# Kernel tuning notes

Hardware: AMD Instinct MI355X
Metric: run time of the kernel (lower is better)

Reference implementation:

```python
import jax, jax.numpy as jnp
import numpy as np

B, N, MAX_V = 256, 16384, 64

def setup_inputs() -> dict:
    key = jax.random.key(0)
    ks = jax.random.split(key, 11)
    s = 0.02
    x = jax.random.normal(ks[0], (B, N, 5), dtype=jnp.float32)
    W1 = jax.random.normal(ks[1], (2, 32), dtype=jnp.float32) * s
    b1 = jnp.zeros((32,), jnp.float32)
    W2 = jax.random.normal(ks[2], (32, 64), dtype=jnp.float32) * s
    b2 = jnp.zeros((64,), jnp.float32)
    W3 = jax.random.normal(ks[3], (201, 256), dtype=jnp.float32) * s
    b3 = jnp.zeros((256,), jnp.float32)
    W4 = jax.random.normal(ks[4], (256, 128), dtype=jnp.float32) * s
    b4 = jnp.zeros((128,), jnp.float32)
    W5 = jax.random.normal(ks[5], (128, MAX_V * 4), dtype=jnp.float32) * s
    # existence-logit biases initialized to -2.0 (indices i*4+3)
    b5 = jnp.zeros((MAX_V * 4,), jnp.float32).at[jnp.arange(MAX_V) * 4 + 3].set(-2.0)
    return {"x": x, "W1": W1, "b1": b1, "W2": W2, "b2": b2,
            "W3": W3, "b3": b3, "W4": W4, "b4": b4, "W5": W5, "b5": b5}

def _pca_align(coords):
    # coords: [B,N,3]
    n = coords.shape[1]
    centroid = coords.mean(axis=1, keepdims=True)          # [B,1,3]
    centered = coords - centroid                           # [B,N,3]
    cov = jnp.einsum('bni,bnj->bij', centered, centered) / n
    evals, evecs = jnp.linalg.eigh(cov)                    # ascending
    evals = evals[:, ::-1]                                 # descending
    evecs = evecs[:, :, ::-1]
    # det sign fix on 3rd column
    det = jnp.linalg.det(evecs)
    evecs = evecs.at[:, :, 2].multiply(jnp.where(det < 0, -1.0, 1.0)[:, None])
    # deterministic sign: each axis points toward side with more mass (vectorized)
    proj = jnp.einsum('bnd,bde->bne', centered, evecs)     # [B,N,3]
    pos = (proj > 0).sum(axis=1)
    neg = (proj < 0).sum(axis=1)
    sign = jnp.where(neg > pos, -1.0, 1.0)                 # [B,3]
    evecs = evecs * sign[:, None, :]
    aligned = jnp.einsum('bnd,bde->bne', centered, evecs)  # [B,N,3]
    eig_norm = evals / (evals.sum(axis=1, keepdims=True) + 1e-8)
    extents = aligned.max(axis=1) - aligned.min(axis=1)    # [B,3]
    pca_features = jnp.concatenate([eig_norm, extents, centroid[:, 0]], axis=1)  # [B,9]
    return aligned, pca_features, evecs, centroid

def reference(x, W1, b1, W2, b2, W3, b3, W4, b4, W5, b5):
    coords = x[:, :, :3]
    sem = x[:, :, 3:]                                      # [B,N,2]
    aligned, pca_features, rot, centroid = _pca_align(coords)
    # per-point MLP
    pf = jax.nn.relu(sem @ W1 + b1)
    pf = jax.nn.relu(pf @ W2 + b2)                         # [B,N,64]
    gmax = pf.max(axis=1)
    gavg = pf.mean(axis=1)
    gstd = jnp.std(pf, axis=1, ddof=1)                     # torch.std is unbiased
    g = jnp.concatenate([gmax, gavg, gstd, pca_features], axis=1)  # [B,201]
    h = jax.nn.relu(g @ W3 + b3)
    h = jax.nn.relu(h @ W4 + b4)
    out = (h @ W5 + b5).reshape(x.shape[0], MAX_V, 4)      # [B,64,4]
    return out
```

## Files before the change

kernel.cpp:

```cpp
#include <hip/hip_runtime.h>
#include <math.h>

#define BATCH 256
#define NPTS  16384
#define TPB   256

#define P1_CHUNKS     8
#define P1_PTS_BLOCK  (NPTS / P1_CHUNKS)
#define P1_ITERS      8

#define PART_STRIDE 256

typedef __bf16 bf16x8  __attribute__((ext_vector_type(8)));
typedef float  floatx4 __attribute__((ext_vector_type(4)));

__global__ __launch_bounds__(TPB, 4)
void pass1_kernel(const float* __restrict__ x, const float* __restrict__ W1,
                  const float* __restrict__ b1, const float* __restrict__ W2,
                  const float* __restrict__ b2, float* __restrict__ ws) {
    const int b     = blockIdx.x;
    const int chunk = blockIdx.y;
    const int tid   = threadIdx.x;
    const int lane  = tid & 63;
    const int wave  = tid >> 6;
    const int quad  = lane >> 4;
    const int l15   = lane & 15;

    bf16x8 Bf[4];
    float  b2n[4];
#pragma unroll
    for (int t = 0; t < 4; ++t) {
        int n = t * 16 + l15;
#pragma unroll
        for (int j = 0; j < 8; ++j)
            Bf[t][j] = (__bf16)W2[(quad * 8 + j) * 64 + n];
        b2n[t] = b2[n];
    }
    float w1a[8], w1b[8], b1r[8];
#pragma unroll
    for (int j = 0; j < 8; ++j) {
        int jj = quad * 8 + j;
        w1a[j] = W1[jj];
        w1b[j] = W1[32 + jj];
        b1r[j] = b1[jj];
    }

    float vmax[4] = {0.f, 0.f, 0.f, 0.f};
    float vsum[4] = {0.f, 0.f, 0.f, 0.f};
    float vsq[4]  = {0.f, 0.f, 0.f, 0.f};
    float mo[9];
#pragma unroll
    for (int j = 0; j < 9; ++j) mo[j] = 0.f;

    const float* xb = x + ((size_t)b * NPTS + (size_t)chunk * P1_PTS_BLOCK) * 5;

    for (int it = 0; it < P1_ITERS; ++it) {
        const int pbase = wave * (P1_ITERS * 64) + it * 64;
        const float* p = xb + (size_t)(pbase + lane) * 5;
        float c0 = p[0], c1 = p[1], c2 = p[2], s0 = p[3], s1 = p[4];
        mo[0] += c0; mo[1] += c1; mo[2] += c2;
        mo[3] = fmaf(c0, c0, mo[3]); mo[4] = fmaf(c0, c1, mo[4]); mo[5] = fmaf(c0, c2, mo[5]);
        mo[6] = fmaf(c1, c1, mo[6]); mo[7] = fmaf(c1, c2, mo[7]); mo[8] = fmaf(c2, c2, mo[8]);

#pragma unroll
        for (int g = 0; g < 4; ++g) {
            int src = g * 16 + l15;
            float gs0 = __shfl(s0, src);
            float gs1 = __shfl(s1, src);
            bf16x8 Af;
#pragma unroll
            for (int j = 0; j < 8; ++j) {
                float v = fmaf(gs0, w1a[j], fmaf(gs1, w1b[j], b1r[j]));
                Af[j] = (__bf16)fmaxf(v, 0.f);
            }
#pragma unroll
            for (int t = 0; t < 4; ++t) {
                floatx4 C = {b2n[t], b2n[t], b2n[t], b2n[t]};
                C = __builtin_amdgcn_mfma_f32_16x16x32_bf16(Af, Bf[t], C, 0, 0, 0);
#pragma unroll
                for (int r = 0; r < 4; ++r) {
                    float v = fmaxf(C[r], 0.f);
                    vmax[t] = fmaxf(vmax[t], v);
                    vsum[t] += v;
                    vsq[t]  = fmaf(v, v, vsq[t]);
                }
            }
        }
    }

#pragma unroll
    for (int t = 0; t < 4; ++t) {
        vmax[t] = fmaxf(vmax[t], __shfl_xor(vmax[t], 16));
        vmax[t] = fmaxf(vmax[t], __shfl_xor(vmax[t], 32));
        vsum[t] += __shfl_xor(vsum[t], 16);
        vsum[t] += __shfl_xor(vsum[t], 32);
        vsq[t]  += __shfl_xor(vsq[t], 16);
        vsq[t]  += __shfl_xor(vsq[t], 32);
    }
#pragma unroll
    for (int j = 0; j < 9; ++j) {
        float v = mo[j];
#pragma unroll
        for (int o = 32; o > 0; o >>= 1) v += __shfl_xor(v, o);
        mo[j] = v;
    }

    __shared__ float red[4][201];
    if (quad == 0) {
#pragma unroll
        for (int t = 0; t < 4; ++t) {
            red[wave][t * 16 + l15]       = vmax[t];
            red[wave][64 + t * 16 + l15]  = vsum[t];
            red[wave][128 + t * 16 + l15] = vsq[t];
        }
    }
    if (lane == 0) {
#pragma unroll
        for (int j = 0; j < 9; ++j) red[wave][192 + j] = mo[j];
    }
    __syncthreads();

    if (tid < 201) {
        float v0 = red[0][tid], v1 = red[1][tid], v2 = red[2][tid], v3 = red[3][tid];
        float r = (tid < 64) ? fmaxf(fmaxf(v0, v1), fmaxf(v2, v3))
                             : (v0 + v1) + (v2 + v3);
        ws[(size_t)(b * P1_CHUNKS + chunk) * PART_STRIDE + tid] = r;
    }
}

__global__ __launch_bounds__(TPB)
void mid_kernel(const float* __restrict__ x,
                const float* __restrict__ W3, const float* __restrict__ b3,
                const float* __restrict__ W4, const float* __restrict__ b4,
                const float* __restrict__ W5, const float* __restrict__ b5,
                const float* __restrict__ ws, float* __restrict__ out) {
    const int b = blockIdx.x, t = threadIdx.x;
    const int lane = t & 63, wave = t >> 6;

    __shared__ float comb[201];
    __shared__ float eg[15];
    __shared__ float redmm[4][8];
    __shared__ float g[224];
    __shared__ float h1[256];
    __shared__ float h2[128];

    if (t < 201) {
        const float* base = ws + (size_t)b * P1_CHUNKS * PART_STRIDE + t;
        float acc = base[0];
        if (t < 64) {
#pragma unroll
            for (int i = 1; i < P1_CHUNKS; ++i) acc = fmaxf(acc, base[i * PART_STRIDE]);
        } else {
#pragma unroll
            for (int i = 1; i < P1_CHUNKS; ++i) acc += base[i * PART_STRIDE];
        }
        comb[t] = acc;
    }
    __syncthreads();

    if (t == 0) {
        const float n = (float)NPTS;
        float mx = comb[192] / n, my = comb[193] / n, mz = comb[194] / n;
        float A[3][3];
        A[0][0] = comb[195] / n - mx * mx; A[0][1] = comb[196] / n - mx * my;
        A[0][2] = comb[197] / n - mx * mz;
        A[1][1] = comb[198] / n - my * my; A[1][2] = comb[199] / n - my * mz;
        A[2][2] = comb[200] / n - mz * mz;
        A[1][0] = A[0][1]; A[2][0] = A[0][2]; A[2][1] = A[1][2];
        float V[3][3] = {{1, 0, 0}, {0, 1, 0}, {0, 0, 1}};
        const int PP[3] = {0, 0, 1};
        const int QQ[3] = {1, 2, 2};
        for (int sweep = 0; sweep < 7; ++sweep) {
            for (int r3 = 0; r3 < 3; ++r3) {
                int p = PP[r3], q = QQ[r3];
                float apq = A[p][q];
                if (fabsf(apq) < 1e-35f) continue;
                float theta = (A[q][q] - A[p][p]) / (2.0f * apq);
                float tt = 1.0f / (fabsf(theta) + sqrtf(fmaf(theta, theta, 1.0f)));
                if (theta < 0.0f) tt = -tt;
                float c = 1.0f / sqrtf(fmaf(tt, tt, 1.0f)), s = tt * c;
                float apq_t = tt * apq;
                A[p][p] -= apq_t;
                A[q][q] += apq_t;
                A[p][q] = A[q][p] = 0.0f;
                for (int r = 0; r < 3; ++r) {
                    if (r != p && r != q) {
                        float arp = A[r][p], arq = A[r][q];
                        A[r][p] = A[p][r] = c * arp - s * arq;
                        A[r][q] = A[q][r] = s * arp + c * arq;
                    }
                    float vrp = V[r][p], vrq = V[r][q];
                    V[r][p] = c * vrp - s * vrq;
                    V[r][q] = s * vrp + c * vrq;
                }
            }
        }
        float w[3] = {A[0][0], A[1][1], A[2][2]};
        int i0 = 0, i1 = 1, i2 = 2, sw;
        if (w[i0] < w[i1]) { sw = i0; i0 = i1; i1 = sw; }
        if (w[i0] < w[i2]) { sw = i0; i0 = i2; i2 = sw; }
        if (w[i1] < w[i2]) { sw = i1; i1 = i2; i2 = sw; }
        int idx[3] = {i0, i1, i2};
        for (int e = 0; e < 3; ++e)
            for (int comp = 0; comp < 3; ++comp)
                eg[e * 3 + comp] = V[comp][idx[e]];
        float sum = w[0] + w[1] + w[2] + 1e-8f;
        for (int e = 0; e < 3; ++e) eg[9 + e] = w[idx[e]] / sum;
        eg[12] = mx; eg[13] = my; eg[14] = mz;
    }
    __syncthreads();

    float e0x = eg[0], e0y = eg[1], e0z = eg[2];
    float e1x = eg[3], e1y = eg[4], e1z = eg[5];
    float e2x = eg[6], e2y = eg[7], e2z = eg[8];
    float cx = eg[12], cy = eg[13], cz = eg[14];

    const float* xb = x + (size_t)b * NPTS * 5;
    float mn[3] = {3.4e38f, 3.4e38f, 3.4e38f};
    float mx3[3] = {-3.4e38f, -3.4e38f, -3.4e38f};
#pragma unroll 4
    for (int i = 0; i < NPTS / TPB; ++i) {
        const float* p = xb + (size_t)(i * TPB + t) * 5;
        float c0 = p[0] - cx, c1 = p[1] - cy, c2 = p[2] - cz;
        float p0 = fmaf(c0, e0x, fmaf(c1, e0y, c2 * e0z));
        float p1 = fmaf(c0, e1x, fmaf(c1, e1y, c2 * e1z));
        float p2 = fmaf(c0, e2x, fmaf(c1, e2y, c2 * e2z));
        mn[0] = fminf(mn[0], p0); mx3[0] = fmaxf(mx3[0], p0);
        mn[1] = fminf(mn[1], p1); mx3[1] = fmaxf(mx3[1], p1);
        mn[2] = fminf(mn[2], p2); mx3[2] = fmaxf(mx3[2], p2);
    }
#pragma unroll
    for (int d = 0; d < 3; ++d) {
        float v = mx3[d];
#pragma unroll
        for (int o = 32; o > 0; o >>= 1) v = fmaxf(v, __shfl_xor(v, o));
        if (lane == 0) redmm[wave][d] = v;
        float u = mn[d];
#pragma unroll
        for (int o = 32; o > 0; o >>= 1) u = fminf(u, __shfl_xor(u, o));
        if (lane == 0) redmm[wave][4 + d] = u;
    }
    __syncthreads();

    if (t < 64) {
        g[t] = comb[t];
        float s = comb[64 + t], sq = comb[128 + t];
        float avg = s * (1.0f / NPTS);
        g[64 + t] = avg;
        float var = (sq - s * avg) / (float)(NPTS - 1);
        g[128 + t] = sqrtf(fmaxf(var, 0.f));
    } else if (t < 73) {
        int j = t - 64;
        if (j < 3) {
            g[192 + j] = eg[9 + j];
        } else if (j < 6) {
            int d = j - 3;
            float fmx = fmaxf(fmaxf(redmm[0][d], redmm[1][d]), fmaxf(redmm[2][d], redmm[3][d]));
            float fmn = fminf(fminf(redmm[0][4 + d], redmm[1][4 + d]),
                              fminf(redmm[2][4 + d], redmm[3][4 + d]));
            g[195 + d] = fmx - fmn;
        } else {
            g[198 + (j - 6)] = eg[12 + (j - 6)];
        }
    }
    __syncthreads();

    float a = b3[t];
    for (int j = 0; j < 201; ++j) a = fmaf(g[j], W3[j * 256 + t], a);
    h1[t] = fmaxf(a, 0.f);
    __syncthreads();
    if (t < 128) {
        float a2 = b4[t];
        for (int j = 0; j < 256; ++j) a2 = fmaf(h1[j], W4[j * 128 + t], a2);
        h2[t] = fmaxf(a2, 0.f);
    }
    __syncthreads();
    float o = b5[t];
    for (int j = 0; j < 128; ++j) o = fmaf(h2[j], W5[j * 256 + t], o);
    out[(size_t)b * 256 + t] = o;
}

extern "C" void kernel_launch(void* const* d_in, const int* in_sizes, int n_in,
                              void* d_out, int out_size, void* d_ws, size_t ws_size,
                              hipStream_t stream) {
    const float* x  = (const float*)d_in[0];
    const float* W1 = (const float*)d_in[1];
    const float* b1 = (const float*)d_in[2];
    const float* W2 = (const float*)d_in[3];
    const float* b2 = (const float*)d_in[4];
    const float* W3 = (const float*)d_in[5];
    const float* b3 = (const float*)d_in[6];
    const float* W4 = (const float*)d_in[7];
    const float* b4 = (const float*)d_in[8];
    const float* W5 = (const float*)d_in[9];
    const float* b5 = (const float*)d_in[10];
    float* out = (float*)d_out;
    float* ws  = (float*)d_ws;

    pass1_kernel<<<dim3(BATCH, P1_CHUNKS), TPB, 0, stream>>>(x, W1, b1, W2, b2, ws);
    mid_kernel<<<dim3(BATCH), TPB, 0, stream>>>(x, W3, b3, W4, b4, W5, b5, ws, out);
}
```

Measured before the change: 224.3 us.

## Fuse pass1 and head kernels using last-block-arrives atomic counter per batch

Merges the per-point pass and the per-batch head kernel into one launch: each chunk block writes its partials, bumps a per-batch atomic counter, and the last arriving block does the PCA, extent scan and MLP head. A tiny kernel zeroes the counters first. This removes the wait between the two kernels so head work for one batch can overlap other batches' pass1 blocks. In exchange it adds an extra launch, fences and atomics, and enlarges shared memory and registers in the fused kernel, which may lower occupancy.

```diff
diff --git a/kernel.cpp b/kernel.cpp
--- a/kernel.cpp
+++ b/kernel.cpp
@@ -10,14 +10,23 @@
 #define P1_ITERS      8
 
 #define PART_STRIDE 256
+#define COUNTER_OFF (BATCH * P1_CHUNKS * PART_STRIDE)
 
 typedef __bf16 bf16x8  __attribute__((ext_vector_type(8)));
 typedef float  floatx4 __attribute__((ext_vector_type(4)));
 
+__global__ void init_counters_kernel(unsigned* __restrict__ wsu) {
+    wsu[COUNTER_OFF + threadIdx.x] = 0u;
+}
+
 __global__ __launch_bounds__(TPB, 4)
-void pass1_kernel(const float* __restrict__ x, const float* __restrict__ W1,
+void fused_kernel(const float* __restrict__ x, const float* __restrict__ W1,
                   const float* __restrict__ b1, const float* __restrict__ W2,
-                  const float* __restrict__ b2, float* __restrict__ ws) {
+                  const float* __restrict__ b2,
+                  const float* __restrict__ W3, const float* __restrict__ b3,
+                  const float* __restrict__ W4, const float* __restrict__ b4,
+                  const float* __restrict__ W5, const float* __restrict__ b5,
+                  float* __restrict__ ws, float* __restrict__ out) {
     const int b     = blockIdx.x;
     const int chunk = blockIdx.y;
     const int tid   = threadIdx.x;
@@ -126,17 +135,19 @@
                              : (v0 + v1) + (v2 + v3);
         ws[(size_t)(b * P1_CHUNKS + chunk) * PART_STRIDE + tid] = r;
     }
-}
-
-__global__ __launch_bounds__(TPB)
-void mid_kernel(const float* __restrict__ x,
-                const float* __restrict__ W3, const float* __restrict__ b3,
-                const float* __restrict__ W4, const float* __restrict__ b4,
-                const float* __restrict__ W5, const float* __restrict__ b5,
-                const float* __restrict__ ws, float* __restrict__ out) {
-    const int b = blockIdx.x, t = threadIdx.x;
-    const int lane = t & 63, wave = t >> 6;
-
+
+    __threadfence();
+    __syncthreads();
+    __shared__ unsigned arrival;
+    if (tid == 0) {
+        unsigned* cnt = (unsigned*)ws + COUNTER_OFF + b;
+        arrival = atomicAdd(cnt, 1u);
+    }
+    __syncthreads();
+    if (arrival != P1_CHUNKS - 1) return;
+    __threadfence();
+
+    const int lane2 = tid & 63, wave2 = tid >> 6;
     __shared__ float comb[201];
     __shared__ float eg[15];
     __shared__ float redmm[4][8];
@@ -144,21 +155,21 @@
     __shared__ float h1[256];
     __shared__ float h2[128];
 
-    if (t < 201) {
-        const float* base = ws + (size_t)b * P1_CHUNKS * PART_STRIDE + t;
+    if (tid < 201) {
+        volatile const float* base = ws + (size_t)b * P1_CHUNKS * PART_STRIDE + tid;
         float acc = base[0];
-        if (t < 64) {
+        if (tid < 64) {
 #pragma unroll
             for (int i = 1; i < P1_CHUNKS; ++i) acc = fmaxf(acc, base[i * PART_STRIDE]);
         } else {
 #pragma unroll
             for (int i = 1; i < P1_CHUNKS; ++i) acc += base[i * PART_STRIDE];
         }
-        comb[t] = acc;
-    }
-    __syncthreads();
-
-    if (t == 0) {
+        comb[tid] = acc;
+    }
+    __syncthreads();
+
+    if (tid == 0) {
         const float n = (float)NPTS;
         float mx = comb[192] / n, my = comb[193] / n, mz = comb[194] / n;
         float A[3][3];
@@ -215,12 +226,12 @@
     float e2x = eg[6], e2y = eg[7], e2z = eg[8];
     float cx = eg[12], cy = eg[13], cz = eg[14];
 
-    const float* xb = x + (size_t)b * NPTS * 5;
+    const float* xf = x + (size_t)b * NPTS * 5;
     float mn[3] = {3.4e38f, 3.4e38f, 3.4e38f};
     float mx3[3] = {-3.4e38f, -3.4e38f, -3.4e38f};
 #pragma unroll 4
     for (int i = 0; i < NPTS / TPB; ++i) {
-        const float* p = xb + (size_t)(i * TPB + t) * 5;
+        const float* p = xf + (size_t)(i * TPB + tid) * 5;
         float c0 = p[0] - cx, c1 = p[1] - cy, c2 = p[2] - cz;
         float p0 = fmaf(c0, e0x, fmaf(c1, e0y, c2 * e0z));
         float p1 = fmaf(c0, e1x, fmaf(c1, e1y, c2 * e1z));
@@ -234,23 +245,23 @@
         float v = mx3[d];
 #pragma unroll
         for (int o = 32; o > 0; o >>= 1) v = fmaxf(v, __shfl_xor(v, o));
-        if (lane == 0) redmm[wave][d] = v;
+        if (lane2 == 0) redmm[wave2][d] = v;
         float u = mn[d];
 #pragma unroll
         for (int o = 32; o > 0; o >>= 1) u = fminf(u, __shfl_xor(u, o));
-        if (lane == 0) redmm[wave][4 + d] = u;
-    }
-    __syncthreads();
-
-    if (t < 64) {
-        g[t] = comb[t];
-        float s = comb[64 + t], sq = comb[128 + t];
+        if (lane2 == 0) redmm[wave2][4 + d] = u;
+    }
+    __syncthreads();
+
+    if (tid < 64) {
+        g[tid] = comb[tid];
+        float s = comb[64 + tid], sq = comb[128 + tid];
         float avg = s * (1.0f / NPTS);
-        g[64 + t] = avg;
+        g[64 + tid] = avg;
         float var = (sq - s * avg) / (float)(NPTS - 1);
-        g[128 + t] = sqrtf(fmaxf(var, 0.f));
-    } else if (t < 73) {
-        int j = t - 64;
+        g[128 + tid] = sqrtf(fmaxf(var, 0.f));
+    } else if (tid < 73) {
+        int j = tid - 64;
         if (j < 3) {
             g[192 + j] = eg[9 + j];
         } else if (j < 6) {
@@ -265,19 +276,19 @@
     }
     __syncthreads();
 
-    float a = b3[t];
-    for (int j = 0; j < 201; ++j) a = fmaf(g[j], W3[j * 256 + t], a);
-    h1[t] = fmaxf(a, 0.f);
-    __syncthreads();
-    if (t < 128) {
-        float a2 = b4[t];
-        for (int j = 0; j < 256; ++j) a2 = fmaf(h1[j], W4[j * 128 + t], a2);
-        h2[t] = fmaxf(a2, 0.f);
-    }
-    __syncthreads();
-    float o = b5[t];
-    for (int j = 0; j < 128; ++j) o = fmaf(h2[j], W5[j * 256 + t], o);
-    out[(size_t)b * 256 + t] = o;
+    float a = b3[tid];
+    for (int j = 0; j < 201; ++j) a = fmaf(g[j], W3[j * 256 + tid], a);
+    h1[tid] = fmaxf(a, 0.f);
+    __syncthreads();
+    if (tid < 128) {
+        float a2 = b4[tid];
+        for (int j = 0; j < 256; ++j) a2 = fmaf(h1[j], W4[j * 128 + tid], a2);
+        h2[tid] = fmaxf(a2, 0.f);
+    }
+    __syncthreads();
+    float o = b5[tid];
+    for (int j = 0; j < 128; ++j) o = fmaf(h2[j], W5[j * 256 + tid], o);
+    out[(size_t)b * 256 + tid] = o;
 }
 
 extern "C" void kernel_launch(void* const* d_in, const int* in_sizes, int n_in,
@@ -297,6 +308,7 @@
     float* out = (float*)d_out;
     float* ws  = (float*)d_ws;
 
-    pass1_kernel<<<dim3(BATCH, P1_CHUNKS), TPB, 0, stream>>>(x, W1, b1, W2, b2, ws);
-    mid_kernel<<<dim3(BATCH), TPB, 0, stream>>>(x, W3, b3, W4, b4, W5, b5, ws, out);
+    init_counters_kernel<<<dim3(1), BATCH, 0, stream>>>((unsigned*)ws);
+    fused_kernel<<<dim3(BATCH, P1_CHUNKS), TPB, 0, stream>>>(
+        x, W1, b1, W2, b2, W3, b3, W4, b4, W5, b5, ws, out);
 }
```

Result: slower. 460.3 us (+105.2%).

## Widen mid kernel to 1024 threads with split-K partial sums for MLP head

Applied to the files above, without the earlier changes.

Raises the mid kernel's block size from 256 to 1024 threads, so the per-batch projection min/max scan over all points uses four times as many threads. The three dense layers are split along the reduction dimension across thread groups, with partial sums reduced through shared memory. The aim is to shorten the serial dot-product chains and the point scan in a kernel that launches only 256 blocks. The cost is extra barriers, extra shared memory and lower per-CU occupancy limits for the larger blocks.

```diff
diff --git a/kernel.cpp b/kernel.cpp
--- a/kernel.cpp
+++ b/kernel.cpp
@@ -4,6 +4,7 @@
 #define BATCH 256
 #define NPTS  16384
 #define TPB   256
+#define MID_TPB 1024
 
 #define P1_CHUNKS     8
 #define P1_PTS_BLOCK  (NPTS / P1_CHUNKS)
@@ -128,7 +129,7 @@
     }
 }
 
-__global__ __launch_bounds__(TPB)
+__global__ __launch_bounds__(MID_TPB)
 void mid_kernel(const float* __restrict__ x,
                 const float* __restrict__ W3, const float* __restrict__ b3,
                 const float* __restrict__ W4, const float* __restrict__ b4,
@@ -139,10 +140,11 @@
 
     __shared__ float comb[201];
     __shared__ float eg[15];
-    __shared__ float redmm[4][8];
+    __shared__ float redmm[16][8];
     __shared__ float g[224];
     __shared__ float h1[256];
     __shared__ float h2[128];
+    __shared__ float part[8][256];
 
     if (t < 201) {
         const float* base = ws + (size_t)b * P1_CHUNKS * PART_STRIDE + t;
@@ -219,8 +221,8 @@
     float mn[3] = {3.4e38f, 3.4e38f, 3.4e38f};
     float mx3[3] = {-3.4e38f, -3.4e38f, -3.4e38f};
 #pragma unroll 4
-    for (int i = 0; i < NPTS / TPB; ++i) {
-        const float* p = xb + (size_t)(i * TPB + t) * 5;
+    for (int i = 0; i < NPTS / MID_TPB; ++i) {
+        const float* p = xb + (size_t)(i * MID_TPB + t) * 5;
         float c0 = p[0] - cx, c1 = p[1] - cy, c2 = p[2] - cz;
         float p0 = fmaf(c0, e0x, fmaf(c1, e0y, c2 * e0z));
         float p1 = fmaf(c0, e1x, fmaf(c1, e1y, c2 * e1z));
@@ -255,9 +257,12 @@
             g[192 + j] = eg[9 + j];
         } else if (j < 6) {
             int d = j - 3;
-            float fmx = fmaxf(fmaxf(redmm[0][d], redmm[1][d]), fmaxf(redmm[2][d], redmm[3][d]));
-            float fmn = fminf(fminf(redmm[0][4 + d], redmm[1][4 + d]),
-                              fminf(redmm[2][4 + d], redmm[3][4 + d]));
+            float fmx = redmm[0][d], fmn = redmm[0][4 + d];
+#pragma unroll
+            for (int w2 = 1; w2 < 16; ++w2) {
+                fmx = fmaxf(fmx, redmm[w2][d]);
+                fmn = fminf(fmn, redmm[w2][4 + d]);
+            }
             g[195 + d] = fmx - fmn;
         } else {
             g[198 + (j - 6)] = eg[12 + (j - 6)];
@@ -265,19 +270,48 @@
     }
     __syncthreads();
 
-    float a = b3[t];
-    for (int j = 0; j < 201; ++j) a = fmaf(g[j], W3[j * 256 + t], a);
-    h1[t] = fmaxf(a, 0.f);
+    {
+        int p = t >> 8, c = t & 255;
+        int j0 = p * 51, j1 = min(201, j0 + 51);
+        float a = 0.f;
+        for (int j = j0; j < j1; ++j) a = fmaf(g[j], W3[j * 256 + c], a);
+        part[p][c] = a;
+    }
+    __syncthreads();
+    if (t < 256) {
+        float a = b3[t] + (part[0][t] + part[1][t]) + (part[2][t] + part[3][t]);
+        h1[t] = fmaxf(a, 0.f);
+    }
+    __syncthreads();
+    {
+        int p = t >> 7, c = t & 127;
+        int j0 = p * 32;
+        float a = 0.f;
+#pragma unroll
+        for (int j = j0; j < j0 + 32; ++j) a = fmaf(h1[j], W4[j * 128 + c], a);
+        part[p][c] = a;
+    }
     __syncthreads();
     if (t < 128) {
-        float a2 = b4[t];
-        for (int j = 0; j < 256; ++j) a2 = fmaf(h1[j], W4[j * 128 + t], a2);
-        h2[t] = fmaxf(a2, 0.f);
-    }
-    __syncthreads();
-    float o = b5[t];
-    for (int j = 0; j < 128; ++j) o = fmaf(h2[j], W5[j * 256 + t], o);
-    out[(size_t)b * 256 + t] = o;
+        float a = b4[t];
+#pragma unroll
+        for (int p = 0; p < 8; ++p) a += part[p][t];
+        h2[t] = fmaxf(a, 0.f);
+    }
+    __syncthreads();
+    {
+        int p = t >> 8, c = t & 255;
+        int j0 = p * 32;
+        float a = 0.f;
+#pragma unroll
+        for (int j = j0; j < j0 + 32; ++j) a = fmaf(h2[j], W5[j * 256 + c], a);
+        part[p][c] = a;
+    }
+    __syncthreads();
+    if (t < 256) {
+        float o = b5[t] + (part[0][t] + part[1][t]) + (part[2][t] + part[3][t]);
+        out[(size_t)b * 256 + t] = o;
+    }
 }
 
 extern "C" void kernel_launch(void* const* d_in, const int* in_sizes, int n_in,
@@ -298,5 +332,5 @@
     float* ws  = (float*)d_ws;
 
     pass1_kernel<<<dim3(BATCH, P1_CHUNKS), TPB, 0, stream>>>(x, W1, b1, W2, b2, ws);
-    mid_kernel<<<dim3(BATCH), TPB, 0, stream>>>(x, W3, b3, W4, b4, W5, b5, ws, out);
+    mid_kernel<<<dim3(BATCH), MID_TPB, 0, stream>>>(x, W3, b3, W4, b4, W5, b5, ws, out);
 }
```

Result: faster. 206.9 us (-7.8%).
